# Kernel tuning notes

Measured on AMD Instinct MI355X. Metric: run time of the kernel, lower is better.

Reference implementation:

```python
import jax, jax.numpy as jnp
import numpy as np

N = 16384

def setup_inputs() -> dict:
    key = jax.random.key(0)
    k1, k2, k3 = jax.random.split(key, 3)
    risk_scores = jax.random.normal(k1, (N,), dtype=jnp.float32)
    survival_times = jax.random.normal(k2, (N,), dtype=jnp.float32)
    # 0/1 event indicator (1 = event observed, 0 = censored)
    events = (jax.random.uniform(k3, (N,)) < 0.5).astype(jnp.float32)
    return {"risk_scores": risk_scores, "survival_times": survival_times, "events": events}

def reference(risk_scores, survival_times, events):
    # Risk-set matrix: R[i, j] = 1 if T[j] >= T[i] (vectorized version of the
    # original O(n^2) double Python loop).
    R = (survival_times[None, :] >= survival_times[:, None]).astype(risk_scores.dtype)  # [n, n]
    exp_theta = jnp.exp(risk_scores)                # [n]
    # sum_j exp(theta_j) * R[i, j]  ->  matvec
    risk_set_sum = R @ exp_theta                    # [n]
    loss = -jnp.mean((risk_scores - jnp.log(risk_set_sum)) * events)
    return loss
```

## Files before the change

### kernel.cpp

```cpp
#include <hip/hip_runtime.h>
#include <math.h>

#define BLOCK 256
#define NB 4096
#define SCAN_T 1024

__global__ void surv_hist(const float* __restrict__ theta,
                          const float* __restrict__ T,
                          int* __restrict__ counts, float* __restrict__ bucketE,
                          float* __restrict__ Earr, int* __restrict__ elemBR, int n) {
    const int i = blockIdx.x * BLOCK + threadIdx.x;
    if (i >= n) return;
    const float Tg = T[i];
    const float E  = expf(theta[i]);
    int b = (int)((Tg + 6.0f) * ((float)NB / 12.0f));
    b = min(max(b, 0), NB - 1);
    const int r = atomicAdd(&counts[b], 1);
    atomicAdd(&bucketE[b], E);
    Earr[i] = E;
    elemBR[i] = (b << 16) | r;
}

__global__ void __launch_bounds__(SCAN_T)
surv_scan(const int* __restrict__ counts, const float* __restrict__ bucketE,
          int* __restrict__ offsets, float* __restrict__ suffixE, int n) {
    __shared__ int   ci[SCAN_T];
    __shared__ float ce[SCAN_T];
    const int t = threadIdx.x;
    const int CH = NB / SCAN_T;
    const int base = t * CH;
    int cl[CH]; float el[CH];
    int cs = 0; float es = 0.f;
#pragma unroll
    for (int k = 0; k < CH; ++k) {
        cl[k] = counts[base + k]; el[k] = bucketE[base + k];
        cs += cl[k]; es += el[k];
    }
    ci[t] = cs; ce[t] = es;
    __syncthreads();
    for (int s = 1; s < SCAN_T; s <<= 1) {
        const int   a = (t >= s)          ? ci[t - s] : 0;
        const float f = (t + s < SCAN_T)  ? ce[t + s] : 0.f;
        __syncthreads();
        ci[t] += a; ce[t] += f;
        __syncthreads();
    }
    int run = ci[t] - cs;
    float rs = ce[t] - es;
#pragma unroll
    for (int k = 0; k < CH; ++k) { offsets[base + k] = run; run += cl[k]; }
#pragma unroll
    for (int k = CH - 1; k >= 0; --k) { rs += el[k]; suffixE[base + k] = rs; }
    if (t == 0) { offsets[NB] = n; suffixE[NB] = 0.f; }
}

__global__ void surv_scatter(const float* __restrict__ T, const float* __restrict__ Earr,
                             const int* __restrict__ elemBR, const int* __restrict__ offsets,
                             float* __restrict__ sortedT, float* __restrict__ sortedE, int n) {
    const int i = blockIdx.x * BLOCK + threadIdx.x;
    if (i >= n) return;
    const int br = elemBR[i];
    const int pos = offsets[br >> 16] + (br & 0xFFFF);
    sortedT[pos] = T[i];
    sortedE[pos] = Earr[i];
}

__global__ void surv_risk_final(const float* __restrict__ theta, const float* __restrict__ T,
                                const float* __restrict__ events,
                                const int* __restrict__ offsets,
                                const float* __restrict__ suffixE,
                                const float* __restrict__ sortedT, const float* __restrict__ sortedE,
                                float* __restrict__ acc, int* __restrict__ done,
                                float* __restrict__ out, int n, int nblocks) {
    __shared__ float red[BLOCK];
    const int tid = threadIdx.x;
    const int i = blockIdx.x * BLOCK + tid;
    float term = 0.f;
    if (i < n) {
        const float Ti = T[i];
        int b = (int)((Ti + 6.0f) * ((float)NB / 12.0f));
        b = min(max(b, 0), NB - 1);
        float risk = suffixE[b + 1];
        const int p0 = offsets[b], p1 = offsets[b + 1];
        for (int p = p0; p < p1; ++p)
            risk += (sortedT[p] >= Ti) ? sortedE[p] : 0.f;
        term = (theta[i] - logf(risk)) * events[i];
    }
    red[tid] = term;
    __syncthreads();
    for (int s = BLOCK / 2; s > 0; s >>= 1) {
        if (tid < s) red[tid] += red[tid + s];
        __syncthreads();
    }
    if (tid == 0) {
        atomicAdd(acc, red[0]);
        __threadfence();
        const int prev = atomicAdd(done, 1);
        if (prev == nblocks - 1) {
            const float total = atomicAdd(acc, 0.0f);
            out[0] = -total / (float)n;
        }
    }
}

__global__ void surv_partial_bf(const float* __restrict__ theta, const float* __restrict__ T,
                                const float* __restrict__ events, float* __restrict__ bsum, int n) {
    __shared__ float red[BLOCK];
    const int tid = threadIdx.x;
    const int i = blockIdx.x * BLOCK + tid;
    float term = 0.f;
    if (i < n) {
        const float Ti = T[i];
        float risk = 0.f;
        for (int j = 0; j < n; ++j)
            risk += (T[j] >= Ti) ? expf(theta[j]) : 0.f;
        term = (theta[i] - logf(risk)) * events[i];
    }
    red[tid] = term;
    __syncthreads();
    for (int s = BLOCK / 2; s > 0; s >>= 1) {
        if (tid < s) red[tid] += red[tid + s];
        __syncthreads();
    }
    if (tid == 0) bsum[blockIdx.x] = red[0];
}

__global__ void surv_final_bf(const float* __restrict__ bsum, float* __restrict__ out,
                              int nblocks, int n) {
    float v = 0.f;
    for (int b = threadIdx.x; b < nblocks; b += 64) v += bsum[b];
    for (int off = 32; off > 0; off >>= 1) v += __shfl_down(v, off, 64);
    if (threadIdx.x == 0) out[0] = -v / (float)n;
}

extern "C" void kernel_launch(void* const* d_in, const int* in_sizes, int n_in,
                              void* d_out, int out_size, void* d_ws, size_t ws_size,
                              hipStream_t stream) {
    const float* theta  = (const float*)d_in[0];
    const float* T      = (const float*)d_in[1];
    const float* events = (const float*)d_in[2];
    float* out = (float*)d_out;
    const int n = in_sizes[0];
    const int nbi = (n + BLOCK - 1) / BLOCK;

    const size_t zero_words = (size_t)2 * NB + 2;
    const size_t need = (zero_words + 2 * (NB + 1) + 4 * (size_t)n) * 4;

    if (n >= (1 << 16) || ws_size < need) {
        float* bsum = (float*)d_ws;
        surv_partial_bf<<<nbi, BLOCK, 0, stream>>>(theta, T, events, bsum, n);
        surv_final_bf<<<1, 64, 0, stream>>>(bsum, out, nbi, n);
        return;
    }

    int*   counts  = (int*)d_ws;
    float* bucketE = (float*)(counts + NB);
    float* acc     = bucketE + NB;
    int*   done    = (int*)(acc + 1);
    int*   offsets = done + 1;
    float* suffixE = (float*)(offsets + NB + 1);
    float* Earr    = suffixE + NB + 1;
    int*   elemBR  = (int*)(Earr + n);
    float* sortedT = (float*)(elemBR + n);
    float* sortedE = sortedT + n;

    hipMemsetAsync(d_ws, 0, zero_words * 4, stream);
    surv_hist<<<nbi, BLOCK, 0, stream>>>(theta, T, counts, bucketE, Earr, elemBR, n);
    surv_scan<<<1, SCAN_T, 0, stream>>>(counts, bucketE, offsets, suffixE, n);
    surv_scatter<<<nbi, BLOCK, 0, stream>>>(T, Earr, elemBR, offsets, sortedT, sortedE, n);
    surv_risk_final<<<nbi, BLOCK, 0, stream>>>(theta, T, events, offsets, suffixE,
                                               sortedT, sortedE, acc, done, out, n, nbi);
}
```

Before: 82.23 us.

## Fuse histogram and scan, replace scatter with fixed-capacity bucket slots

Merges the histogram and suffix-scan kernels using a last-block-done pattern, and removes the separate scatter kernel. Each element now writes (T, exp) directly into a fixed-capacity per-bucket slot array, with an overflow list for buckets holding more than CAP entries. This cuts the pipeline from four launches to two and drops the offsets prefix scan. In exchange, the final kernel scans the whole overflow list per thread, which is costly if many buckets overflow, and the fast path now requires n to be a multiple of the block size.

After: 83.93 us. 2.1% more time.

```diff
diff --git a/kernel.cpp b/kernel.cpp
--- a/kernel.cpp
+++ b/kernel.cpp
@@ -3,87 +3,96 @@
 
 #define BLOCK 256
 #define NB 4096
-#define SCAN_T 1024
+#define CAP 64
 
-__global__ void surv_hist(const float* __restrict__ theta,
-                          const float* __restrict__ T,
-                          int* __restrict__ counts, float* __restrict__ bucketE,
-                          float* __restrict__ Earr, int* __restrict__ elemBR, int n) {
-    const int i = blockIdx.x * BLOCK + threadIdx.x;
-    if (i >= n) return;
-    const float Tg = T[i];
-    const float E  = expf(theta[i]);
+__device__ __forceinline__ int bucket_of(float Tg) {
     int b = (int)((Tg + 6.0f) * ((float)NB / 12.0f));
-    b = min(max(b, 0), NB - 1);
-    const int r = atomicAdd(&counts[b], 1);
-    atomicAdd(&bucketE[b], E);
-    Earr[i] = E;
-    elemBR[i] = (b << 16) | r;
+    return min(max(b, 0), NB - 1);
 }
 
-__global__ void __launch_bounds__(SCAN_T)
-surv_scan(const int* __restrict__ counts, const float* __restrict__ bucketE,
-          int* __restrict__ offsets, float* __restrict__ suffixE, int n) {
-    __shared__ int   ci[SCAN_T];
-    __shared__ float ce[SCAN_T];
+__global__ void __launch_bounds__(BLOCK)
+surv_hist_scan(const float* __restrict__ theta, const float* __restrict__ T,
+               int* __restrict__ counts, float* __restrict__ bucketE,
+               float2* __restrict__ slots, float* __restrict__ ovTE,
+               int* __restrict__ novf, int* __restrict__ done,
+               float* __restrict__ suffixE, int n, int nblocks) {
+    const int i = blockIdx.x * BLOCK + threadIdx.x;
+    if (i < n) {
+        const float Tg = T[i];
+        const float E  = expf(theta[i]);
+        const int b = bucket_of(Tg);
+        const int r = atomicAdd(&counts[b], 1);
+        atomicAdd(&bucketE[b], E);
+        if (r < CAP) {
+            slots[b * CAP + r] = make_float2(Tg, E);
+        } else {
+            const int o = atomicAdd(novf, 1);
+            ovTE[2 * o] = Tg; ovTE[2 * o + 1] = E;
+        }
+    }
+
+    __shared__ int lastFlag;
+    __threadfence();
+    __syncthreads();
+    if (threadIdx.x == 0) {
+        const int prev = atomicAdd(done, 1);
+        lastFlag = (prev == nblocks - 1) ? 1 : 0;
+    }
+    __syncthreads();
+    if (!lastFlag) return;
+
+    __shared__ float ce[BLOCK];
     const int t = threadIdx.x;
-    const int CH = NB / SCAN_T;
+    const int CH = NB / BLOCK;
     const int base = t * CH;
-    int cl[CH]; float el[CH];
-    int cs = 0; float es = 0.f;
+    float el[CH];
+    float es = 0.f;
 #pragma unroll
     for (int k = 0; k < CH; ++k) {
-        cl[k] = counts[base + k]; el[k] = bucketE[base + k];
-        cs += cl[k]; es += el[k];
+        el[k] = atomicAdd(&bucketE[base + k], 0.0f);
+        es += el[k];
     }
-    ci[t] = cs; ce[t] = es;
+    ce[t] = es;
     __syncthreads();
-    for (int s = 1; s < SCAN_T; s <<= 1) {
-        const int   a = (t >= s)          ? ci[t - s] : 0;
-        const float f = (t + s < SCAN_T)  ? ce[t + s] : 0.f;
+    for (int s = 1; s < BLOCK; s <<= 1) {
+        const float f = (t + s < BLOCK) ? ce[t + s] : 0.f;
         __syncthreads();
-        ci[t] += a; ce[t] += f;
+        ce[t] += f;
         __syncthreads();
     }
-    int run = ci[t] - cs;
     float rs = ce[t] - es;
 #pragma unroll
-    for (int k = 0; k < CH; ++k) { offsets[base + k] = run; run += cl[k]; }
-#pragma unroll
     for (int k = CH - 1; k >= 0; --k) { rs += el[k]; suffixE[base + k] = rs; }
-    if (t == 0) { offsets[NB] = n; suffixE[NB] = 0.f; }
+    if (t == 0) suffixE[NB] = 0.f;
 }
 
-__global__ void surv_scatter(const float* __restrict__ T, const float* __restrict__ Earr,
-                             const int* __restrict__ elemBR, const int* __restrict__ offsets,
-                             float* __restrict__ sortedT, float* __restrict__ sortedE, int n) {
-    const int i = blockIdx.x * BLOCK + threadIdx.x;
-    if (i >= n) return;
-    const int br = elemBR[i];
-    const int pos = offsets[br >> 16] + (br & 0xFFFF);
-    sortedT[pos] = T[i];
-    sortedE[pos] = Earr[i];
-}
-
-__global__ void surv_risk_final(const float* __restrict__ theta, const float* __restrict__ T,
-                                const float* __restrict__ events,
-                                const int* __restrict__ offsets,
-                                const float* __restrict__ suffixE,
-                                const float* __restrict__ sortedT, const float* __restrict__ sortedE,
-                                float* __restrict__ acc, int* __restrict__ done,
-                                float* __restrict__ out, int n, int nblocks) {
+__global__ void __launch_bounds__(BLOCK)
+surv_risk_final(const float* __restrict__ theta, const float* __restrict__ T,
+                const float* __restrict__ events,
+                const int* __restrict__ counts, const float* __restrict__ suffixE,
+                const float2* __restrict__ slots, const float* __restrict__ ovTE,
+                const int* __restrict__ novf,
+                float* __restrict__ acc, int* __restrict__ done2,
+                float* __restrict__ out, int n, int nblocks) {
     __shared__ float red[BLOCK];
     const int tid = threadIdx.x;
     const int i = blockIdx.x * BLOCK + tid;
     float term = 0.f;
     if (i < n) {
         const float Ti = T[i];
-        int b = (int)((Ti + 6.0f) * ((float)NB / 12.0f));
-        b = min(max(b, 0), NB - 1);
+        const int b = bucket_of(Ti);
         float risk = suffixE[b + 1];
-        const int p0 = offsets[b], p1 = offsets[b + 1];
-        for (int p = p0; p < p1; ++p)
-            risk += (sortedT[p] >= Ti) ? sortedE[p] : 0.f;
+        const int m = min(counts[b], CAP);
+        const float2* sp = slots + (size_t)b * CAP;
+        for (int p = 0; p < m; ++p) {
+            const float2 te = sp[p];
+            risk += (te.x >= Ti) ? te.y : 0.f;
+        }
+        const int nv = *novf;
+        for (int o = 0; o < nv; ++o) {
+            const float Tj = ovTE[2 * o];
+            if (bucket_of(Tj) == b && Tj >= Ti) risk += ovTE[2 * o + 1];
+        }
         term = (theta[i] - logf(risk)) * events[i];
     }
     red[tid] = term;
@@ -95,7 +104,7 @@
     if (tid == 0) {
         atomicAdd(acc, red[0]);
         __threadfence();
-        const int prev = atomicAdd(done, 1);
+        const int prev = atomicAdd(done2, 1);
         if (prev == nblocks - 1) {
             const float total = atomicAdd(acc, 0.0f);
             out[0] = -total / (float)n;
@@ -143,31 +152,30 @@
     const int n = in_sizes[0];
     const int nbi = (n + BLOCK - 1) / BLOCK;
 
-    const size_t zero_words = (size_t)2 * NB + 2;
-    const size_t need = (zero_words + 2 * (NB + 1) + 4 * (size_t)n) * 4;
+    const size_t zero_words = (size_t)2 * NB + 4;
+    const size_t pre_slots  = zero_words + (NB + 1) + 1;
+    const size_t need = (pre_slots + (size_t)2 * NB * CAP + 2 * (size_t)n) * 4;
 
-    if (n >= (1 << 16) || ws_size < need) {
+    if ((n % BLOCK) != 0 || ws_size < need) {
         float* bsum = (float*)d_ws;
         surv_partial_bf<<<nbi, BLOCK, 0, stream>>>(theta, T, events, bsum, n);
         surv_final_bf<<<1, 64, 0, stream>>>(bsum, out, nbi, n);
         return;
     }
 
-    int*   counts  = (int*)d_ws;
-    float* bucketE = (float*)(counts + NB);
-    float* acc     = bucketE + NB;
-    int*   done    = (int*)(acc + 1);
-    int*   offsets = done + 1;
-    float* suffixE = (float*)(offsets + NB + 1);
-    float* Earr    = suffixE + NB + 1;
-    int*   elemBR  = (int*)(Earr + n);
-    float* sortedT = (float*)(elemBR + n);
-    float* sortedE = sortedT + n;
+    int*    counts  = (int*)d_ws;
+    float*  bucketE = (float*)(counts + NB);
+    float*  acc     = bucketE + NB;
+    int*    done    = (int*)(acc + 1);
+    int*    done2   = done + 1;
+    int*    novf    = done2 + 1;
+    float*  suffixE = (float*)(novf + 1);
+    float2* slots   = (float2*)((float*)d_ws + pre_slots);
+    float*  ovTE    = (float*)(slots + (size_t)NB * CAP);
 
     hipMemsetAsync(d_ws, 0, zero_words * 4, stream);
-    surv_hist<<<nbi, BLOCK, 0, stream>>>(theta, T, counts, bucketE, Earr, elemBR, n);
-    surv_scan<<<1, SCAN_T, 0, stream>>>(counts, bucketE, offsets, suffixE, n);
-    surv_scatter<<<nbi, BLOCK, 0, stream>>>(T, Earr, elemBR, offsets, sortedT, sortedE, n);
-    surv_risk_final<<<nbi, BLOCK, 0, stream>>>(theta, T, events, offsets, suffixE,
-                                               sortedT, sortedE, acc, done, out, n, nbi);
+    surv_hist_scan<<<nbi, BLOCK, 0, stream>>>(theta, T, counts, bucketE, slots,
+                                              ovTE, novf, done, suffixE, n, nbi);
+    surv_risk_final<<<nbi, BLOCK, 0, stream>>>(theta, T, events, counts, suffixE,
+                                               slots, ovTE, novf, acc, done2, out, n, nbi);
 }
```
